# Optimization experiments

Hardware: AMD Instinct MI355X
Metric: run time of the kernel (lower is better)

The kernel has to match this reference:

```python
import jax, jax.numpy as jnp
import numpy as np

N = 50000        # nodes
F = 128          # input feature dim
U = 128          # units (output dim)
E_RAND = 1_600_000  # random edges; N self-loops appended -> E = 1_650_000
LABEL_IDXS = np.array([0, 5, 17, 42], dtype=np.int32)  # label_idxs init arg (indices into F)


def setup_inputs() -> dict:
    key = jax.random.key(0)
    k1, k2, k3, k4, k5 = jax.random.split(key, 5)
    x = jax.random.normal(k1, (1, N, F), dtype=jnp.float32)
    src = jax.random.randint(k2, (E_RAND,), 0, N, dtype=jnp.int32)
    dst = jax.random.randint(k3, (E_RAND,), 0, N, dtype=jnp.int32)
    # append self-loops so the diagonal of A (Adiag term) is nontrivial,
    # matching a normalized Laplacian which always has diagonal entries
    loops = jnp.arange(N, dtype=jnp.int32)
    edge_src = jnp.concatenate([src, loops])
    edge_dst = jnp.concatenate([dst, loops])
    edge_w = jax.random.uniform(k4, (E_RAND + N,), dtype=jnp.float32)
    kernel = jax.random.normal(k5, (F, U), dtype=jnp.float32) * (1.0 / np.sqrt(F))
    bias = jnp.zeros((U,), dtype=jnp.float32)
    return {"x": x, "edge_src": edge_src, "edge_dst": edge_dst,
            "edge_w": edge_w, "kernel": kernel, "bias": bias}


def reference(x, edge_src, edge_dst, edge_w, kernel, bias):
    # x: [1, N, F]; sparse A given as COO edges (edge_src=row i, edge_dst=col j, edge_w=A[i,j])
    n = x.shape[1]
    xs = x[0]  # [N, F]
    # A @ X  (sparse matmul via gather + segment_sum)
    agg = jax.ops.segment_sum(edge_w[:, None] * xs[edge_dst], edge_src, num_segments=n)  # [N, F]
    # diag(A): entries where row == col
    diag = jax.ops.segment_sum(jnp.where(edge_src == edge_dst, edge_w, jnp.float32(0.0)),
                               edge_src, num_segments=n)  # [N]
    # B = sum_{i in label_idxs} e_i e_i^T is a diagonal 0/1 selector on feature columns,
    # so (Adiag @ X) @ B == diag[:,None] * (X * mask)
    mask = jnp.zeros((xs.shape[1],), xs.dtype).at[jnp.asarray(LABEL_IDXS)].set(1.0)  # [F]
    h = agg - diag[:, None] * (xs * mask)  # [N, F]
    out = jax.nn.relu(h @ kernel + bias)   # [N, U]
    return out[None]  # [1, N, U]
```

## Files before the change

kernel.cpp:

```cpp
#include <hip/hip_runtime.h>

#define FDIM 128
#define UDIM 128
#define BROWS 256
#define CAP   9728
#define TILE  4096
#define EPT   16

typedef __attribute__((ext_vector_type(8))) short short8;
typedef __attribute__((ext_vector_type(4))) float floatx4;

__device__ inline unsigned int round_bf16_bits(float a) {
  unsigned int ua = __float_as_uint(a);
  ua += 0x7fffu + ((ua >> 16) & 1u);
  return ua & 0xffff0000u;
}
__device__ inline unsigned int pack_bf16(float a, float b) {
  unsigned int ua = __float_as_uint(a);
  unsigned int ub = __float_as_uint(b);
  ua += 0x7fffu + ((ua >> 16) & 1u);
  ub += 0x7fffu + ((ub >> 16) & 1u);
  return (ua >> 16) | (ub & 0xffff0000u);
}

__global__ __launch_bounds__(256) void bin_edges(
    const int* __restrict__ src, const int* __restrict__ dst,
    const float* __restrict__ w, int* __restrict__ cursor,
    unsigned int* __restrict__ binned_dstw, unsigned char* __restrict__ binned_src,
    float* __restrict__ diag, int E, int NB) {
  __shared__ int scnt[256];
  __shared__ int sbase[256];
  __shared__ int scur[256];
  int t = threadIdx.x;
  scnt[t] = 0; scur[t] = 0;
  __syncthreads();

  uint2 pay[EPT];
  int e0 = blockIdx.x * TILE;
  #pragma unroll
  for (int j = 0; j < EPT; ++j) {
    int e = e0 + j * 256 + t;
    if (e < E) {
      int s = src[e];
      int d = dst[e];
      float wv = w[e];
      if (s == d) atomicAdd(&diag[s], wv);
      pay[j].x = round_bf16_bits(wv) | (unsigned int)d;
      pay[j].y = (unsigned int)s;
      atomicAdd(&scnt[s >> 8], 1);
    } else {
      pay[j].y = 0xffffffffu;
    }
  }
  __syncthreads();

  if (t < NB) {
    int c = scnt[t];
    if (c) sbase[t] = t * CAP + atomicAdd(&cursor[t], c);
  }
  __syncthreads();

  #pragma unroll
  for (int j = 0; j < EPT; ++j) {
    if (pay[j].y != 0xffffffffu) {
      int b = pay[j].y >> 8;
      int r = atomicAdd(&scur[b], 1);
      int pos = sbase[b] + r;
      if (pos < (b + 1) * CAP) {
        binned_dstw[pos] = pay[j].x;
        binned_src[pos] = (unsigned char)(pay[j].y & 255u);
      }
    }
  }
}

__global__ __launch_bounds__(256) void sort_bucket(
    const unsigned int* __restrict__ binned_dstw,
    const unsigned char* __restrict__ binned_src,
    const int* __restrict__ cursor,
    int* __restrict__ rs, unsigned int* __restrict__ meta, int N, int NB) {
  __shared__ unsigned short skey[CAP];
  __shared__ int kcnt[1024];
  __shared__ int pscan[256];
  int b = blockIdx.x;
  int t = threadIdx.x;
  int row0 = b * BROWS;
  int nrows = N - row0; if (nrows > BROWS) nrows = BROWS;
  int base_in = b * CAP;

  int cb = 0;
  if (t < NB) { cb = cursor[t]; if (cb > CAP) cb = CAP; }
  pscan[t] = cb;
  __syncthreads();
  int v = cb;
  for (int off = 1; off < 256; off <<= 1) {
    int add = (t >= off) ? pscan[t - off] : 0;
    __syncthreads();
    v += add; pscan[t] = v;
    __syncthreads();
  }
  int cntE = cursor[b]; if (cntE > CAP) cntE = CAP;
  int base_out = pscan[b] - cntE;
  if (b == 0 && t == 0) rs[N] = pscan[NB - 1];

  kcnt[t] = 0; kcnt[256 + t] = 0; kcnt[512 + t] = 0; kcnt[768 + t] = 0;
  __syncthreads();

  for (int e = t; e < cntE; e += 256) {
    unsigned int dw = binned_dstw[base_in + e];
    int sl = binned_src[base_in + e];
    int key = (sl << 2) | (int)(((dw & 0xffffu) * 41u) >> 19);
    skey[e] = (unsigned short)key;
    atomicAdd(&kcnt[key], 1);
  }
  __syncthreads();

  int c0 = kcnt[4 * t], c1 = kcnt[4 * t + 1], c2 = kcnt[4 * t + 2], c3 = kcnt[4 * t + 3];
  int local = c0 + c1 + c2 + c3;
  pscan[t] = local;
  __syncthreads();
  int v2 = local;
  for (int off = 1; off < 256; off <<= 1) {
    int add = (t >= off) ? pscan[t - off] : 0;
    __syncthreads();
    v2 += add; pscan[t] = v2;
    __syncthreads();
  }
  int excl = base_out + v2 - local;
  if (t < nrows) rs[row0 + t] = excl;
  kcnt[4 * t] = excl;
  kcnt[4 * t + 1] = excl + c0;
  kcnt[4 * t + 2] = excl + c0 + c1;
  kcnt[4 * t + 3] = excl + c0 + c1 + c2;
  __syncthreads();

  for (int e = t; e < cntE; e += 256) {
    int key = skey[e];
    int pos = atomicAdd(&kcnt[key], 1);
    meta[pos] = binned_dstw[base_in + e];
  }
}

__global__ __launch_bounds__(64) void prep_kfrag(
    const float* __restrict__ K, uint4* __restrict__ kfrag) {
  int lane = threadIdx.x;
  int n = (blockIdx.x >> 2) * 16 + (lane & 15);
  int k0 = (blockIdx.x & 3) * 32 + (lane >> 4) * 8;
  unsigned int p[4];
  #pragma unroll
  for (int j = 0; j < 4; ++j) {
    float a = K[(size_t)(k0 + 2 * j) * UDIM + n];
    float b = K[(size_t)(k0 + 2 * j + 1) * UDIM + n];
    p[j] = pack_bf16(a, b);
  }
  kfrag[(size_t)blockIdx.x * 64 + lane] = make_uint4(p[0], p[1], p[2], p[3]);
}

__global__ __launch_bounds__(256) void gemm_y_mfma(
    const float* __restrict__ x, const uint4* __restrict__ kfrag,
    unsigned short* __restrict__ Ybf, int N) {
  __shared__ unsigned short sX[64][136];
  int t = threadIdx.x;
  int r0 = blockIdx.x * 64;

  #pragma unroll
  for (int i = 0; i < 8; ++i) {
    int li = i * 256 + t;
    int row = li >> 5;
    int col4 = (li & 31) * 4;
    int gr = r0 + row; if (gr > N - 1) gr = N - 1;
    float4 v = *(const float4*)(x + (size_t)gr * FDIM + col4);
    *(uint2*)(&sX[row][col4]) = make_uint2(pack_bf16(v.x, v.y), pack_bf16(v.z, v.w));
  }
  __syncthreads();

  int wave = t >> 6, lane = t & 63;
  int m = lane & 15, q = lane >> 4;

  short8 bf[2][4];
  #pragma unroll
  for (int c = 0; c < 2; ++c)
    #pragma unroll
    for (int ks = 0; ks < 4; ++ks)
      bf[c][ks] = *(const short8*)&kfrag[(size_t)((2 * wave + c) * 4 + ks) * 64 + lane];

  floatx4 acc[4][2];
  #pragma unroll
  for (int rt = 0; rt < 4; ++rt)
    #pragma unroll
    for (int c = 0; c < 2; ++c)
      acc[rt][c] = (floatx4){0.f, 0.f, 0.f, 0.f};

  #pragma unroll
  for (int ks = 0; ks < 4; ++ks) {
    #pragma unroll
    for (int rt = 0; rt < 4; ++rt) {
      short8 af = *(const short8*)&sX[rt * 16 + m][ks * 32 + q * 8];
      acc[rt][0] = __builtin_amdgcn_mfma_f32_16x16x32_bf16(af, bf[0][ks], acc[rt][0], 0, 0, 0);
      acc[rt][1] = __builtin_amdgcn_mfma_f32_16x16x32_bf16(af, bf[1][ks], acc[rt][1], 0, 0, 0);
    }
  }

  #pragma unroll
  for (int rt = 0; rt < 4; ++rt) {
    #pragma unroll
    for (int c = 0; c < 2; ++c) {
      int col = (2 * wave + c) * 16 + m;
      #pragma unroll
      for (int reg = 0; reg < 4; ++reg) {
        int r = r0 + rt * 16 + q * 4 + reg;
        if (r < N)
          Ybf[(size_t)r * UDIM + col] =
              (unsigned short)(round_bf16_bits(acc[rt][c][reg]) >> 16);
      }
    }
  }
}

__global__ __launch_bounds__(256) void gather_out(
    const unsigned short* __restrict__ Ybf, const int* __restrict__ rs,
    const unsigned int* __restrict__ meta,
    const float* __restrict__ diag, const float* __restrict__ x,
    const float* __restrict__ K, const float* __restrict__ bias,
    float* __restrict__ out, int N) {
  int r = blockIdx.x * 8 + (threadIdx.x >> 5);
  if (r >= N) return;
  int sub = threadIdx.x & 31;
  int base = rs[r], end = rs[r + 1];
  int len = end - base;

  unsigned int m0 = 0, m1 = 0;
  if (sub < len) m0 = __builtin_nontemporal_load(&meta[base + sub]);
  if (32 + sub < len) m1 = __builtin_nontemporal_load(&meta[base + 32 + sub]);

  float4 acc = {0.f, 0.f, 0.f, 0.f};
  int nk = len < 64 ? len : 64;
  int i = 0;
  for (; i + 8 <= nk; i += 8) {
    unsigned int msel = (i & 32) ? m1 : m0;
    unsigned int mi[8];
    #pragma unroll
    for (int j = 0; j < 8; ++j) mi[j] = __shfl(msel, (i + j) & 31, 32);
    uint2 pk[8];
    #pragma unroll
    for (int j = 0; j < 8; ++j)
      pk[j] = *(const uint2*)(Ybf + (size_t)(mi[j] & 0xffffu) * UDIM + sub * 4);
    #pragma unroll
    for (int j = 0; j < 8; ++j) {
      float wj = __uint_as_float(mi[j] & 0xffff0000u);
      acc.x += wj * __uint_as_float(pk[j].x << 16);
      acc.y += wj * __uint_as_float(pk[j].x & 0xffff0000u);
      acc.z += wj * __uint_as_float(pk[j].y << 16);
      acc.w += wj * __uint_as_float(pk[j].y & 0xffff0000u);
    }
  }
  for (; i < nk; ++i) {
    unsigned int mi = __shfl((i & 32) ? m1 : m0, i & 31, 32);
    float wj = __uint_as_float(mi & 0xffff0000u);
    uint2 pk = *(const uint2*)(Ybf + (size_t)(mi & 0xffffu) * UDIM + sub * 4);
    acc.x += wj * __uint_as_float(pk.x << 16);
    acc.y += wj * __uint_as_float(pk.x & 0xffff0000u);
    acc.z += wj * __uint_as_float(pk.y << 16);
    acc.w += wj * __uint_as_float(pk.y & 0xffff0000u);
  }
  for (int k0 = base + 64; k0 < end; k0 += 32) {
    int nk2 = end - k0; if (nk2 > 32) nk2 = 32;
    unsigned int m2 = 0;
    if (sub < nk2) m2 = __builtin_nontemporal_load(&meta[k0 + sub]);
    for (int j = 0; j < nk2; ++j) {
      unsigned int mi = __shfl(m2, j, 32);
      float wj = __uint_as_float(mi & 0xffff0000u);
      uint2 pk = *(const uint2*)(Ybf + (size_t)(mi & 0xffffu) * UDIM + sub * 4);
      acc.x += wj * __uint_as_float(pk.x << 16);
      acc.y += wj * __uint_as_float(pk.x & 0xffff0000u);
      acc.z += wj * __uint_as_float(pk.y << 16);
      acc.w += wj * __uint_as_float(pk.y & 0xffff0000u);
    }
  }

  float dg = diag[r];
  const int lf[4] = {0, 5, 17, 42};
  #pragma unroll
  for (int tt = 0; tt < 4; ++tt) {
    float c = dg * x[(size_t)r * FDIM + lf[tt]];
    float4 k4 = *(const float4*)(K + lf[tt] * UDIM + sub * 4);
    acc.x -= c * k4.x; acc.y -= c * k4.y;
    acc.z -= c * k4.z; acc.w -= c * k4.w;
  }

  float4 b4 = *(const float4*)(bias + sub * 4);
  acc.x = fmaxf(acc.x + b4.x, 0.f);
  acc.y = fmaxf(acc.y + b4.y, 0.f);
  acc.z = fmaxf(acc.z + b4.z, 0.f);
  acc.w = fmaxf(acc.w + b4.w, 0.f);
  *(float4*)(out + (size_t)r * UDIM + sub * 4) = acc;
}

extern "C" void kernel_launch(void* const* d_in, const int* in_sizes, int n_in,
                              void* d_out, int out_size, void* d_ws, size_t ws_size,
                              hipStream_t stream) {
  const float* x    = (const float*)d_in[0];
  const int*   esrc = (const int*)d_in[1];
  const int*   edst = (const int*)d_in[2];
  const float* ew   = (const float*)d_in[3];
  const float* K    = (const float*)d_in[4];
  const float* bias = (const float*)d_in[5];
  float* out = (float*)d_out;

  const int N = in_sizes[0] / FDIM;
  const int E = in_sizes[1];
  const int NB = (N + BROWS - 1) / BROWS;

  char* p = (char*)d_ws;
  unsigned short* Ybf = (unsigned short*)p; p += (size_t)N * UDIM * 2;
  float* diag  = (float*)p;         p += (size_t)N * 4;
  int*   cursor = (int*)p;          p += (size_t)NB * 4;
  int*   rs    = (int*)p;           p += (size_t)(N + 1) * 4;
  uint4* kfrag = (uint4*)p;         p += (size_t)32 * 64 * 16;
  unsigned int* binned_dstw = (unsigned int*)p; p += (size_t)NB * CAP * 4;
  unsigned int* meta = (unsigned int*)p;        p += (size_t)E * 4;
  unsigned char* binned_src = (unsigned char*)p; p += (size_t)NB * CAP;

  hipMemsetAsync(diag, 0, (size_t)(N + NB) * 4, stream);

  prep_kfrag<<<32, 64, 0, stream>>>(K, kfrag);
  bin_edges<<<(E + TILE - 1) / TILE, 256, 0, stream>>>(
      esrc, edst, ew, cursor, binned_dstw, binned_src, diag, E, NB);
  sort_bucket<<<NB, 256, 0, stream>>>(binned_dstw, binned_src, cursor,
                                      rs, meta, N, NB);

  gemm_y_mfma<<<(N + 63) / 64, 256, 0, stream>>>(x, kfrag, Ybf, N);
  gather_out<<<(N + 7) / 8, 256, 0, stream>>>(Ybf, rs, meta, diag, x, K, bias, out, N);
}
```

Measured before the change: 207.8 us.

## Fuse all GCN stages into one persistent cooperative kernel with grid syncs

Replaces the memset and five separate kernel launches with a single cooperative persistent kernel. The stages are separated by grid-wide syncs, and the blocks loop over work units. Edge binning and the X·K GEMM tiles now share one phase, so they can overlap. This removes launch gaps and idle tails between kernels. In exchange it adds grid-sync costs, occupancy limits from the larger shared buffer, and host-side occupancy queries on each call. The nontemporal meta loads are also dropped.

```diff
diff --git a/kernel.cpp b/kernel.cpp
--- a/kernel.cpp
+++ b/kernel.cpp
@@ -1,4 +1,7 @@
 #include <hip/hip_runtime.h>
+#include <hip/hip_cooperative_groups.h>
+
+namespace cg = cooperative_groups;
 
 #define FDIM 128
 #define UDIM 128
@@ -10,6 +13,15 @@
 typedef __attribute__((ext_vector_type(8))) short short8;
 typedef __attribute__((ext_vector_type(4))) float floatx4;
 
+struct Params {
+  const float* x; const int* esrc; const int* edst; const float* ew;
+  const float* K; const float* bias; float* out;
+  float* diag; int* cursor; int* rs; uint4* kfrag;
+  unsigned int* binned_dstw; unsigned char* binned_src;
+  unsigned int* meta; unsigned short* Ybf;
+  int N, E, NB, nbin, ngemm;
+};
+
 __device__ inline unsigned int round_bf16_bits(float a) {
   unsigned int ua = __float_as_uint(a);
   ua += 0x7fffu + ((ua >> 16) & 1u);
@@ -23,28 +35,24 @@
   return (ua >> 16) | (ub & 0xffff0000u);
 }
 
-__global__ __launch_bounds__(256) void bin_edges(
-    const int* __restrict__ src, const int* __restrict__ dst,
-    const float* __restrict__ w, int* __restrict__ cursor,
-    unsigned int* __restrict__ binned_dstw, unsigned char* __restrict__ binned_src,
-    float* __restrict__ diag, int E, int NB) {
-  __shared__ int scnt[256];
-  __shared__ int sbase[256];
-  __shared__ int scur[256];
+__device__ void bin_tile(const Params& P, int u, char* smem) {
+  int* scnt  = (int*)smem;
+  int* sbase = (int*)(smem + 1024);
+  int* scur  = (int*)(smem + 2048);
   int t = threadIdx.x;
   scnt[t] = 0; scur[t] = 0;
   __syncthreads();
 
   uint2 pay[EPT];
-  int e0 = blockIdx.x * TILE;
+  int e0 = u * TILE;
   #pragma unroll
   for (int j = 0; j < EPT; ++j) {
     int e = e0 + j * 256 + t;
-    if (e < E) {
-      int s = src[e];
-      int d = dst[e];
-      float wv = w[e];
-      if (s == d) atomicAdd(&diag[s], wv);
+    if (e < P.E) {
+      int s = P.esrc[e];
+      int d = P.edst[e];
+      float wv = P.ew[e];
+      if (s == d) atomicAdd(&P.diag[s], wv);
       pay[j].x = round_bf16_bits(wv) | (unsigned int)d;
       pay[j].y = (unsigned int)s;
       atomicAdd(&scnt[s >> 8], 1);
@@ -54,9 +62,9 @@
   }
   __syncthreads();
 
-  if (t < NB) {
+  if (t < P.NB) {
     int c = scnt[t];
-    if (c) sbase[t] = t * CAP + atomicAdd(&cursor[t], c);
+    if (c) sbase[t] = t * CAP + atomicAdd(&P.cursor[t], c);
   }
   __syncthreads();
 
@@ -67,109 +75,25 @@
       int r = atomicAdd(&scur[b], 1);
       int pos = sbase[b] + r;
       if (pos < (b + 1) * CAP) {
-        binned_dstw[pos] = pay[j].x;
-        binned_src[pos] = (unsigned char)(pay[j].y & 255u);
+        P.binned_dstw[pos] = pay[j].x;
+        P.binned_src[pos] = (unsigned char)(pay[j].y & 255u);
       }
     }
   }
 }
 
-__global__ __launch_bounds__(256) void sort_bucket(
-    const unsigned int* __restrict__ binned_dstw,
-    const unsigned char* __restrict__ binned_src,
-    const int* __restrict__ cursor,
-    int* __restrict__ rs, unsigned int* __restrict__ meta, int N, int NB) {
-  __shared__ unsigned short skey[CAP];
-  __shared__ int kcnt[1024];
-  __shared__ int pscan[256];
-  int b = blockIdx.x;
+__device__ void gemm_tile(const Params& P, int g, char* smem) {
+  unsigned short (*sX)[136] = (unsigned short (*)[136])smem;
   int t = threadIdx.x;
-  int row0 = b * BROWS;
-  int nrows = N - row0; if (nrows > BROWS) nrows = BROWS;
-  int base_in = b * CAP;
-
-  int cb = 0;
-  if (t < NB) { cb = cursor[t]; if (cb > CAP) cb = CAP; }
-  pscan[t] = cb;
-  __syncthreads();
-  int v = cb;
-  for (int off = 1; off < 256; off <<= 1) {
-    int add = (t >= off) ? pscan[t - off] : 0;
-    __syncthreads();
-    v += add; pscan[t] = v;
-    __syncthreads();
-  }
-  int cntE = cursor[b]; if (cntE > CAP) cntE = CAP;
-  int base_out = pscan[b] - cntE;
-  if (b == 0 && t == 0) rs[N] = pscan[NB - 1];
-
-  kcnt[t] = 0; kcnt[256 + t] = 0; kcnt[512 + t] = 0; kcnt[768 + t] = 0;
-  __syncthreads();
-
-  for (int e = t; e < cntE; e += 256) {
-    unsigned int dw = binned_dstw[base_in + e];
-    int sl = binned_src[base_in + e];
-    int key = (sl << 2) | (int)(((dw & 0xffffu) * 41u) >> 19);
-    skey[e] = (unsigned short)key;
-    atomicAdd(&kcnt[key], 1);
-  }
-  __syncthreads();
-
-  int c0 = kcnt[4 * t], c1 = kcnt[4 * t + 1], c2 = kcnt[4 * t + 2], c3 = kcnt[4 * t + 3];
-  int local = c0 + c1 + c2 + c3;
-  pscan[t] = local;
-  __syncthreads();
-  int v2 = local;
-  for (int off = 1; off < 256; off <<= 1) {
-    int add = (t >= off) ? pscan[t - off] : 0;
-    __syncthreads();
-    v2 += add; pscan[t] = v2;
-    __syncthreads();
-  }
-  int excl = base_out + v2 - local;
-  if (t < nrows) rs[row0 + t] = excl;
-  kcnt[4 * t] = excl;
-  kcnt[4 * t + 1] = excl + c0;
-  kcnt[4 * t + 2] = excl + c0 + c1;
-  kcnt[4 * t + 3] = excl + c0 + c1 + c2;
-  __syncthreads();
-
-  for (int e = t; e < cntE; e += 256) {
-    int key = skey[e];
-    int pos = atomicAdd(&kcnt[key], 1);
-    meta[pos] = binned_dstw[base_in + e];
-  }
-}
-
-__global__ __launch_bounds__(64) void prep_kfrag(
-    const float* __restrict__ K, uint4* __restrict__ kfrag) {
-  int lane = threadIdx.x;
-  int n = (blockIdx.x >> 2) * 16 + (lane & 15);
-  int k0 = (blockIdx.x & 3) * 32 + (lane >> 4) * 8;
-  unsigned int p[4];
-  #pragma unroll
-  for (int j = 0; j < 4; ++j) {
-    float a = K[(size_t)(k0 + 2 * j) * UDIM + n];
-    float b = K[(size_t)(k0 + 2 * j + 1) * UDIM + n];
-    p[j] = pack_bf16(a, b);
-  }
-  kfrag[(size_t)blockIdx.x * 64 + lane] = make_uint4(p[0], p[1], p[2], p[3]);
-}
-
-__global__ __launch_bounds__(256) void gemm_y_mfma(
-    const float* __restrict__ x, const uint4* __restrict__ kfrag,
-    unsigned short* __restrict__ Ybf, int N) {
-  __shared__ unsigned short sX[64][136];
-  int t = threadIdx.x;
-  int r0 = blockIdx.x * 64;
+  int r0 = g * 64;
 
   #pragma unroll
   for (int i = 0; i < 8; ++i) {
     int li = i * 256 + t;
     int row = li >> 5;
     int col4 = (li & 31) * 4;
-    int gr = r0 + row; if (gr > N - 1) gr = N - 1;
-    float4 v = *(const float4*)(x + (size_t)gr * FDIM + col4);
+    int gr = r0 + row; if (gr > P.N - 1) gr = P.N - 1;
+    float4 v = *(const float4*)(P.x + (size_t)gr * FDIM + col4);
     *(uint2*)(&sX[row][col4]) = make_uint2(pack_bf16(v.x, v.y), pack_bf16(v.z, v.w));
   }
   __syncthreads();
@@ -182,7 +106,7 @@
   for (int c = 0; c < 2; ++c)
     #pragma unroll
     for (int ks = 0; ks < 4; ++ks)
-      bf[c][ks] = *(const short8*)&kfrag[(size_t)((2 * wave + c) * 4 + ks) * 64 + lane];
+      bf[c][ks] = *(const short8*)&P.kfrag[(size_t)((2 * wave + c) * 4 + ks) * 64 + lane];
 
   floatx4 acc[4][2];
   #pragma unroll
@@ -209,29 +133,86 @@
       #pragma unroll
       for (int reg = 0; reg < 4; ++reg) {
         int r = r0 + rt * 16 + q * 4 + reg;
-        if (r < N)
-          Ybf[(size_t)r * UDIM + col] =
+        if (r < P.N)
+          P.Ybf[(size_t)r * UDIM + col] =
               (unsigned short)(round_bf16_bits(acc[rt][c][reg]) >> 16);
       }
     }
   }
 }
 
-__global__ __launch_bounds__(256) void gather_out(
-    const unsigned short* __restrict__ Ybf, const int* __restrict__ rs,
-    const unsigned int* __restrict__ meta,
-    const float* __restrict__ diag, const float* __restrict__ x,
-    const float* __restrict__ K, const float* __restrict__ bias,
-    float* __restrict__ out, int N) {
-  int r = blockIdx.x * 8 + (threadIdx.x >> 5);
-  if (r >= N) return;
+__device__ void sort_bucket_dev(const Params& P, int b, char* smem) {
+  unsigned short* skey = (unsigned short*)smem;
+  int* kcnt  = (int*)(smem + 19456);
+  int* pscan = (int*)(smem + 23552);
+  int t = threadIdx.x;
+  int row0 = b * BROWS;
+  int nrows = P.N - row0; if (nrows > BROWS) nrows = BROWS;
+  int base_in = b * CAP;
+
+  int cb = 0;
+  if (t < P.NB) { cb = P.cursor[t]; if (cb > CAP) cb = CAP; }
+  pscan[t] = cb;
+  __syncthreads();
+  int v = cb;
+  for (int off = 1; off < 256; off <<= 1) {
+    int add = (t >= off) ? pscan[t - off] : 0;
+    __syncthreads();
+    v += add; pscan[t] = v;
+    __syncthreads();
+  }
+  int cntE = P.cursor[b]; if (cntE > CAP) cntE = CAP;
+  int base_out = pscan[b] - cntE;
+  if (b == 0 && t == 0) P.rs[P.N] = pscan[P.NB - 1];
+
+  kcnt[t] = 0; kcnt[256 + t] = 0; kcnt[512 + t] = 0; kcnt[768 + t] = 0;
+  __syncthreads();
+
+  for (int e = t; e < cntE; e += 256) {
+    unsigned int dw = P.binned_dstw[base_in + e];
+    int sl = P.binned_src[base_in + e];
+    int key = (sl << 2) | (int)(((dw & 0xffffu) * 41u) >> 19);
+    skey[e] = (unsigned short)key;
+    atomicAdd(&kcnt[key], 1);
+  }
+  __syncthreads();
+
+  int c0 = kcnt[4 * t], c1 = kcnt[4 * t + 1], c2 = kcnt[4 * t + 2], c3 = kcnt[4 * t + 3];
+  int local = c0 + c1 + c2 + c3;
+  pscan[t] = local;
+  __syncthreads();
+  int v2 = local;
+  for (int off = 1; off < 256; off <<= 1) {
+    int add = (t >= off) ? pscan[t - off] : 0;
+    __syncthreads();
+    v2 += add; pscan[t] = v2;
+    __syncthreads();
+  }
+  int excl = base_out + v2 - local;
+  if (t < nrows) P.rs[row0 + t] = excl;
+  kcnt[4 * t] = excl;
+  kcnt[4 * t + 1] = excl + c0;
+  kcnt[4 * t + 2] = excl + c0 + c1;
+  kcnt[4 * t + 3] = excl + c0 + c1 + c2;
+  __syncthreads();
+
+  for (int e = t; e < cntE; e += 256) {
+    int key = skey[e];
+    int pos = atomicAdd(&kcnt[key], 1);
+    P.meta[pos] = P.binned_dstw[base_in + e];
+  }
+}
+
+__device__ void gather_octet(const Params& P, int o) {
+  int r = o * 8 + (threadIdx.x >> 5);
+  if (r >= P.N) return;
   int sub = threadIdx.x & 31;
-  int base = rs[r], end = rs[r + 1];
+  int base = P.rs[r], end = P.rs[r + 1];
   int len = end - base;
 
   unsigned int m0 = 0, m1 = 0;
-  if (sub < len) m0 = __builtin_nontemporal_load(&meta[base + sub]);
-  if (32 + sub < len) m1 = __builtin_nontemporal_load(&meta[base + 32 + sub]);
+  if (sub < len) m0 = P.meta[base + sub];
+  if (32 + sub < len) m1 = P.meta[base + 32 + sub];
 
   float4 acc = {0.f, 0.f, 0.f, 0.f};
   int nk = len < 64 ? len : 64;
@@ -244,7 +225,7 @@
     uint2 pk[8];
     #pragma unroll
     for (int j = 0; j < 8; ++j)
-      pk[j] = *(const uint2*)(Ybf + (size_t)(mi[j] & 0xffffu) * UDIM + sub * 4);
+      pk[j] = *(const uint2*)(P.Ybf + (size_t)(mi[j] & 0xffffu) * UDIM + sub * 4);
     #pragma unroll
     for (int j = 0; j < 8; ++j) {
       float wj = __uint_as_float(mi[j] & 0xffff0000u);
@@ -257,7 +238,7 @@
   for (; i < nk; ++i) {
     unsigned int mi = __shfl((i & 32) ? m1 : m0, i & 31, 32);
     float wj = __uint_as_float(mi & 0xffff0000u);
-    uint2 pk = *(const uint2*)(Ybf + (size_t)(mi & 0xffffu) * UDIM + sub * 4);
+    uint2 pk = *(const uint2*)(P.Ybf + (size_t)(mi & 0xffffu) * UDIM + sub * 4);
     acc.x += wj * __uint_as_float(pk.x << 16);
     acc.y += wj * __uint_as_float(pk.x & 0xffff0000u);
     acc.z += wj * __uint_as_float(pk.y << 16);
@@ -266,11 +247,11 @@
   for (int k0 = base + 64; k0 < end; k0 += 32) {
     int nk2 = end - k0; if (nk2 > 32) nk2 = 32;
     unsigned int m2 = 0;
-    if (sub < nk2) m2 = __builtin_nontemporal_load(&meta[k0 + sub]);
+    if (sub < nk2) m2 = P.meta[k0 + sub];
     for (int j = 0; j < nk2; ++j) {
       unsigned int mi = __shfl(m2, j, 32);
       float wj = __uint_as_float(mi & 0xffff0000u);
-      uint2 pk = *(const uint2*)(Ybf + (size_t)(mi & 0xffffu) * UDIM + sub * 4);
+      uint2 pk = *(const uint2*)(P.Ybf + (size_t)(mi & 0xffffu) * UDIM + sub * 4);
       acc.x += wj * __uint_as_float(pk.x << 16);
       acc.y += wj * __uint_as_float(pk.x & 0xffff0000u);
       acc.z += wj * __uint_as_float(pk.y << 16);
@@ -278,22 +259,68 @@
     }
   }
 
-  float dg = diag[r];
+  float dg = P.diag[r];
   const int lf[4] = {0, 5, 17, 42};
   #pragma unroll
   for (int tt = 0; tt < 4; ++tt) {
-    float c = dg * x[(size_t)r * FDIM + lf[tt]];
-    float4 k4 = *(const float4*)(K + lf[tt] * UDIM + sub * 4);
+    float c = dg * P.x[(size_t)r * FDIM + lf[tt]];
+    float4 k4 = *(const float4*)(P.K + lf[tt] * UDIM + sub * 4);
     acc.x -= c * k4.x; acc.y -= c * k4.y;
     acc.z -= c * k4.z; acc.w -= c * k4.w;
   }
 
-  float4 b4 = *(const float4*)(bias + sub * 4);
+  float4 b4 = *(const float4*)(P.bias + sub * 4);
   acc.x = fmaxf(acc.x + b4.x, 0.f);
   acc.y = fmaxf(acc.y + b4.y, 0.f);
   acc.z = fmaxf(acc.z + b4.z, 0.f);
   acc.w = fmaxf(acc.w + b4.w, 0.f);
-  *(float4*)(out + (size_t)r * UDIM + sub * 4) = acc;
+  *(float4*)(P.out + (size_t)r * UDIM + sub * 4) = acc;
+}
+
+__global__ __launch_bounds__(256) void fused_gcn(Params P) {
+  cg::grid_group grid = cg::this_grid();
+  __shared__ alignas(16) char smem[24576];
+  int t = threadIdx.x;
+  int gid = blockIdx.x * 256 + t;
+  int gtot = gridDim.x * 256;
+
+  for (int i = gid; i < P.N + P.NB; i += gtot) ((int*)P.diag)[i] = 0;
+  for (int i = gid; i < 2048; i += gtot) {
+    int lane = i & 63, bb = i >> 6;
+    int n = (bb >> 2) * 16 + (lane & 15);
+    int k0 = (bb & 3) * 32 + (lane >> 4) * 8;
+    unsigned int pq[4];
+    #pragma unroll
+    for (int j = 0; j < 4; ++j) {
+      float a = P.K[(size_t)(k0 + 2 * j) * UDIM + n];
+      float b = P.K[(size_t)(k0 + 2 * j + 1) * UDIM + n];
+      pq[j] = pack_bf16(a, b);
+    }
+    P.kfrag[i] = make_uint4(pq[0], pq[1], pq[2], pq[3]);
+  }
+  __threadfence();
+  grid.sync();
+
+  int nunits = P.nbin + P.ngemm;
+  for (int u = blockIdx.x; u < nunits; u += gridDim.x) {
+    __syncthreads();
+    if (u < P.nbin) bin_tile(P, u, smem);
+    else gemm_tile(P, u - P.nbin, smem);
+  }
+  __threadfence();
+  grid.sync();
+
+  for (int b = blockIdx.x; b < P.NB; b += gridDim.x) {
+    __syncthreads();
+    sort_bucket_dev(P, b, smem);
+  }
+  __threadfence();
+  grid.sync();
+
+  int nrg = (P.N + 7) / 8;
+  for (int o = blockIdx.x; o < nrg; o += gridDim.x) {
+    gather_octet(P, o);
+  }
 }
 
 extern "C" void kernel_launch(void* const* d_in, const int* in_sizes, int n_in,
@@ -321,14 +348,23 @@
   unsigned int* meta = (unsigned int*)p;        p += (size_t)E * 4;
   unsigned char* binned_src = (unsigned char*)p; p += (size_t)NB * CAP;
 
-  hipMemsetAsync(diag, 0, (size_t)(N + NB) * 4, stream);
-
-  prep_kfrag<<<32, 64, 0, stream>>>(K, kfrag);
-  bin_edges<<<(E + TILE - 1) / TILE, 256, 0, stream>>>(
-      esrc, edst, ew, cursor, binned_dstw, binned_src, diag, E, NB);
-  sort_bucket<<<NB, 256, 0, stream>>>(binned_dstw, binned_src, cursor,
-                                      rs, meta, N, NB);
-
-  gemm_y_mfma<<<(N + 63) / 64, 256, 0, stream>>>(x, kfrag, Ybf, N);
-  gather_out<<<(N + 7) / 8, 256, 0, stream>>>(Ybf, rs, meta, diag, x, K, bias, out, N);
-}
+  Params P;
+  P.x = x; P.esrc = esrc; P.edst = edst; P.ew = ew; P.K = K; P.bias = bias;
+  P.out = out; P.diag = diag; P.cursor = cursor; P.rs = rs; P.kfrag = kfrag;
+  P.binned_dstw = binned_dstw; P.binned_src = binned_src; P.meta = meta;
+  P.Ybf = Ybf;
+  P.N = N; P.E = E; P.NB = NB;
+  P.nbin = (E + TILE - 1) / TILE;
+  P.ngemm = (N + 63) / 64;
+
+  int numCU = 0;
+  hipDeviceGetAttribute(&numCU, hipDeviceAttributeMultiprocessorCount, 0);
+  int occ = 0;
+  hipOccupancyMaxActiveBlocksPerMultiprocessor(&occ, fused_gcn, 256, 0);
+  if (occ < 1) occ = 1;
+  if (numCU < 1) numCU = 256;
+  int G = numCU * occ;
+
+  void* args[] = {&P};
+  hipLaunchCooperativeKernel((void*)fused_gcn, dim3(G), dim3(256), args, 0, stream);
+}
```

Measured after the change: 561.8 us. +170.4%, slower.

## Halve bucket size and fuse sort with GEMM in one launch

Applied to the files above, without the earlier changes.

Halves the row buckets from 256 to 128 rows, giving twice as many sort blocks with smaller LDS footprints and more parallelism. The bucket sort and the bf16 MFMA GEMM become one kernel that dispatches by block index, so the two independent stages run concurrently. The memset and kfrag prep are merged into one small prep kernel, which cuts launch count. The sort also caches the dst/weight words in LDS so the scatter pass does not reread global memory. In exchange the binning kernel uses 512 shared-memory counters and a two-bucket-per-thread scan, and bucket overflow is more likely with the smaller CAP.

```diff
diff --git a/kernel.cpp b/kernel.cpp
--- a/kernel.cpp
+++ b/kernel.cpp
@@ -2,10 +2,10 @@
 
 #define FDIM 128
 #define UDIM 128
-#define BROWS 256
-#define CAP   9728
-#define TILE  4096
-#define EPT   16
+#define BROWS 128
+#define CAP   4800
+#define TILE  2048
+#define EPT   8
 
 typedef __attribute__((ext_vector_type(8))) short short8;
 typedef __attribute__((ext_vector_type(4))) float floatx4;
@@ -23,16 +23,38 @@
   return (ua >> 16) | (ub & 0xffff0000u);
 }
 
+__global__ __launch_bounds__(256) void prep(
+    const float* __restrict__ K, uint4* __restrict__ kfrag,
+    int* __restrict__ zbase, int zcount) {
+  int gid = blockIdx.x * 256 + threadIdx.x;
+  if (gid < 2048) {
+    int lane = gid & 63, bb = gid >> 6;
+    int n = (bb >> 2) * 16 + (lane & 15);
+    int k0 = (bb & 3) * 32 + (lane >> 4) * 8;
+    unsigned int pq[4];
+    #pragma unroll
+    for (int j = 0; j < 4; ++j) {
+      float a = K[(size_t)(k0 + 2 * j) * UDIM + n];
+      float b = K[(size_t)(k0 + 2 * j + 1) * UDIM + n];
+      pq[j] = pack_bf16(a, b);
+    }
+    kfrag[gid] = make_uint4(pq[0], pq[1], pq[2], pq[3]);
+  }
+  int gtot = gridDim.x * 256;
+  for (int i = gid; i < zcount; i += gtot) zbase[i] = 0;
+}
+
 __global__ __launch_bounds__(256) void bin_edges(
     const int* __restrict__ src, const int* __restrict__ dst,
     const float* __restrict__ w, int* __restrict__ cursor,
     unsigned int* __restrict__ binned_dstw, unsigned char* __restrict__ binned_src,
     float* __restrict__ diag, int E, int NB) {
-  __shared__ int scnt[256];
-  __shared__ int sbase[256];
-  __shared__ int scur[256];
+  __shared__ int scnt[512];
+  __shared__ int sbase[512];
+  __shared__ int scur[512];
   int t = threadIdx.x;
-  scnt[t] = 0; scur[t] = 0;
+  scnt[t] = 0; scnt[256 + t] = 0;
+  scur[t] = 0; scur[256 + t] = 0;
   __syncthreads();
 
   uint2 pay[EPT];
@@ -47,76 +69,83 @@
       if (s == d) atomicAdd(&diag[s], wv);
       pay[j].x = round_bf16_bits(wv) | (unsigned int)d;
       pay[j].y = (unsigned int)s;
-      atomicAdd(&scnt[s >> 8], 1);
+      atomicAdd(&scnt[s >> 7], 1);
     } else {
       pay[j].y = 0xffffffffu;
     }
   }
   __syncthreads();
 
-  if (t < NB) {
-    int c = scnt[t];
-    if (c) sbase[t] = t * CAP + atomicAdd(&cursor[t], c);
+  for (int b = t; b < NB; b += 256) {
+    int c = scnt[b];
+    if (c) sbase[b] = b * CAP + atomicAdd(&cursor[b], c);
   }
   __syncthreads();
 
   #pragma unroll
   for (int j = 0; j < EPT; ++j) {
     if (pay[j].y != 0xffffffffu) {
-      int b = pay[j].y >> 8;
+      int b = pay[j].y >> 7;
       int r = atomicAdd(&scur[b], 1);
       int pos = sbase[b] + r;
       if (pos < (b + 1) * CAP) {
         binned_dstw[pos] = pay[j].x;
-        binned_src[pos] = (unsigned char)(pay[j].y & 255u);
+        binned_src[pos] = (unsigned char)(pay[j].y & 127u);
       }
     }
   }
 }
 
-__global__ __launch_bounds__(256) void sort_bucket(
-    const unsigned int* __restrict__ binned_dstw,
-    const unsigned char* __restrict__ binned_src,
-    const int* __restrict__ cursor,
-    int* __restrict__ rs, unsigned int* __restrict__ meta, int N, int NB) {
-  __shared__ unsigned short skey[CAP];
-  __shared__ int kcnt[1024];
-  __shared__ int pscan[256];
-  int b = blockIdx.x;
+__device__ void sort_dev(int b, const unsigned int* __restrict__ binned_dstw,
+                         const unsigned char* __restrict__ binned_src,
+                         const int* __restrict__ cursor, int* __restrict__ rs,
+                         unsigned int* __restrict__ meta, int N, int NB,
+                         char* smem) {
+  unsigned int* sdstw = (unsigned int*)smem;
+  unsigned short* skey = (unsigned short*)(smem + 19200);
+  int* kcnt  = (int*)(smem + 28800);
+  int* pscan = (int*)(smem + 30848);
+  int* sBase = (int*)(smem + 31872);
   int t = threadIdx.x;
   int row0 = b * BROWS;
   int nrows = N - row0; if (nrows > BROWS) nrows = BROWS;
   int base_in = b * CAP;
 
-  int cb = 0;
-  if (t < NB) { cb = cursor[t]; if (cb > CAP) cb = CAP; }
-  pscan[t] = cb;
-  __syncthreads();
-  int v = cb;
+  int b2 = 2 * t;
+  int ca = 0, cb = 0;
+  if (b2 < NB)     { ca = cursor[b2];     if (ca > CAP) ca = CAP; }
+  if (b2 + 1 < NB) { cb = cursor[b2 + 1]; if (cb > CAP) cb = CAP; }
+  int pairv = ca + cb;
+  pscan[t] = pairv;
+  __syncthreads();
+  int v = pairv;
   for (int off = 1; off < 256; off <<= 1) {
     int add = (t >= off) ? pscan[t - off] : 0;
     __syncthreads();
     v += add; pscan[t] = v;
     __syncthreads();
   }
+  if (t == (b >> 1)) *sBase = v - pairv + ((b & 1) ? ca : 0);
+  if (b == 0 && t == 255) rs[N] = v;
+
+  kcnt[t] = 0; kcnt[256 + t] = 0;
+  __syncthreads();
+
+  int base_out = *sBase;
   int cntE = cursor[b]; if (cntE > CAP) cntE = CAP;
-  int base_out = pscan[b] - cntE;
-  if (b == 0 && t == 0) rs[N] = pscan[NB - 1];
-
-  kcnt[t] = 0; kcnt[256 + t] = 0; kcnt[512 + t] = 0; kcnt[768 + t] = 0;
-  __syncthreads();
 
   for (int e = t; e < cntE; e += 256) {
     unsigned int dw = binned_dstw[base_in + e];
     int sl = binned_src[base_in + e];
     int key = (sl << 2) | (int)(((dw & 0xffffu) * 41u) >> 19);
+    sdstw[e] = dw;
     skey[e] = (unsigned short)key;
     atomicAdd(&kcnt[key], 1);
   }
   __syncthreads();
 
-  int c0 = kcnt[4 * t], c1 = kcnt[4 * t + 1], c2 = kcnt[4 * t + 2], c3 = kcnt[4 * t + 3];
-  int local = c0 + c1 + c2 + c3;
+  int k0 = kcnt[2 * t], k1 = kcnt[2 * t + 1];
+  int local = k0 + k1;
   pscan[t] = local;
   __syncthreads();
   int v2 = local;
@@ -127,41 +156,25 @@
     __syncthreads();
   }
   int excl = base_out + v2 - local;
-  if (t < nrows) rs[row0 + t] = excl;
-  kcnt[4 * t] = excl;
-  kcnt[4 * t + 1] = excl + c0;
-  kcnt[4 * t + 2] = excl + c0 + c1;
-  kcnt[4 * t + 3] = excl + c0 + c1 + c2;
+  kcnt[2 * t] = excl;
+  kcnt[2 * t + 1] = excl + k0;
+  __syncthreads();
+  if (t < nrows) rs[row0 + t] = kcnt[4 * t];
   __syncthreads();
 
   for (int e = t; e < cntE; e += 256) {
     int key = skey[e];
     int pos = atomicAdd(&kcnt[key], 1);
-    meta[pos] = binned_dstw[base_in + e];
-  }
-}
-
-__global__ __launch_bounds__(64) void prep_kfrag(
-    const float* __restrict__ K, uint4* __restrict__ kfrag) {
-  int lane = threadIdx.x;
-  int n = (blockIdx.x >> 2) * 16 + (lane & 15);
-  int k0 = (blockIdx.x & 3) * 32 + (lane >> 4) * 8;
-  unsigned int p[4];
-  #pragma unroll
-  for (int j = 0; j < 4; ++j) {
-    float a = K[(size_t)(k0 + 2 * j) * UDIM + n];
-    float b = K[(size_t)(k0 + 2 * j + 1) * UDIM + n];
-    p[j] = pack_bf16(a, b);
-  }
-  kfrag[(size_t)blockIdx.x * 64 + lane] = make_uint4(p[0], p[1], p[2], p[3]);
-}
-
-__global__ __launch_bounds__(256) void gemm_y_mfma(
-    const float* __restrict__ x, const uint4* __restrict__ kfrag,
-    unsigned short* __restrict__ Ybf, int N) {
-  __shared__ unsigned short sX[64][136];
+    meta[pos] = sdstw[e];
+  }
+}
+
+__device__ void gemm_dev(int g, const float* __restrict__ x,
+                         const uint4* __restrict__ kfrag,
+                         unsigned short* __restrict__ Ybf, int N, char* smem) {
+  unsigned short (*sX)[136] = (unsigned short (*)[136])smem;
   int t = threadIdx.x;
-  int r0 = blockIdx.x * 64;
+  int r0 = g * 64;
 
   #pragma unroll
   for (int i = 0; i < 8; ++i) {
@@ -215,6 +228,20 @@
       }
     }
   }
+}
+
+__global__ __launch_bounds__(256) void sort_gemm(
+    const unsigned int* __restrict__ binned_dstw,
+    const unsigned char* __restrict__ binned_src,
+    const int* __restrict__ cursor, int* __restrict__ rs,
+    unsigned int* __restrict__ meta,
+    const float* __restrict__ x, const uint4* __restrict__ kfrag,
+    unsigned short* __restrict__ Ybf, int N, int NB, int nsort) {
+  __shared__ alignas(16) char smem[31888];
+  if (blockIdx.x < (unsigned)nsort)
+    sort_dev(blockIdx.x, binned_dstw, binned_src, cursor, rs, meta, N, NB, smem);
+  else
+    gemm_dev(blockIdx.x - nsort, x, kfrag, Ybf, N, smem);
 }
 
 __global__ __launch_bounds__(256) void gather_out(
@@ -321,14 +348,13 @@
   unsigned int* meta = (unsigned int*)p;        p += (size_t)E * 4;
   unsigned char* binned_src = (unsigned char*)p; p += (size_t)NB * CAP;
 
-  hipMemsetAsync(diag, 0, (size_t)(N + NB) * 4, stream);
-
-  prep_kfrag<<<32, 64, 0, stream>>>(K, kfrag);
+  const int nsort = NB;
+  const int ngemm = (N + 63) / 64;
+
+  prep<<<128, 256, 0, stream>>>(K, kfrag, (int*)diag, N + NB);
   bin_edges<<<(E + TILE - 1) / TILE, 256, 0, stream>>>(
       esrc, edst, ew, cursor, binned_dstw, binned_src, diag, E, NB);
-  sort_bucket<<<NB, 256, 0, stream>>>(binned_dstw, binned_src, cursor,
-                                      rs, meta, N, NB);
-
-  gemm_y_mfma<<<(N + 63) / 64, 256, 0, stream>>>(x, kfrag, Ybf, N);
+  sort_gemm<<<nsort + ngemm, 256, 0, stream>>>(
+      binned_dstw, binned_src, cursor, rs, meta, x, kfrag, Ybf, N, NB, nsort);
   gather_out<<<(N + 7) / 8, 256, 0, stream>>>(Ybf, rs, meta, diag, x, K, bias, out, N);
 }
```

New measurement: 197.2 us. -5.1%, faster.
